# Performance work log

Measured on AMD Instinct MI355X. Metric: run time of the kernel, lower is better.

The kernel has to match this reference:

```python
import jax, jax.numpy as jnp
import numpy as np

N, NC, G, C = 80000, 8000, 16, 5
E, ES = 160000, 80000
NUM_OPS, OP_E, OP_F, CFG_F, H = 120, 32, 140, 18, 32
ALPHA = 0.2  # tf.nn.leaky_relu default slope

seg = jax.ops.segment_sum

def lrelu(x):
    return jnp.where(x >= 0, x, ALPHA * x)

def l2norm(x):
    s = jnp.sum(x * x, axis=-1, keepdims=True)
    return x * jax.lax.rsqrt(jnp.maximum(s, 1e-12))

def setup_inputs():
    k = jax.random.split(jax.random.key(0), 20)
    p = lambda i, shp, s=0.1: jax.random.normal(k[i], shp, jnp.float32) * s
    d_in = CFG_F + OP_F + OP_E  # 190: concat(config, op feats, op embed)
    d_gc = CFG_F + H            # 50: concat(config, hidden)
    return {
        'op_feats': jax.random.normal(k[0], (N, OP_F), jnp.float32),
        'config_feats': jax.random.normal(k[1], (NC, C, CFG_F), jnp.float32),
        'op_ids': jax.random.randint(k[2], (N,), 0, NUM_OPS),
        'selected': jax.random.randint(k[3], (N,), 0, 2) == 1,
        'feed_src': jax.random.randint(k[4], (E,), 0, N),
        'feed_dst': jax.random.randint(k[5], (E,), 0, N),
        'sfeed_src': jax.random.randint(k[6], (ES,), 0, N),
        'sfeed_dst': jax.random.randint(k[7], (ES,), 0, N),
        'config_src': jnp.arange(NC),
        'config_dst': jax.random.randint(k[8], (NC,), 0, N),
        'sconfig_src': jnp.arange(NC),
        'sconfig_dst': jax.random.randint(k[9], (NC,), 0, N),
        'op_gid': (jnp.arange(N) * G) // N,
        'cfg_gid': (jnp.arange(NC) * G) // NC,
        'emb': p(10, (NUM_OPS, OP_E), 1.0),
        'pre_w1': p(11, (d_in, H)), 'pre_b1': jnp.zeros((H,), jnp.float32),
        'pre_w2': p(12, (H, H)), 'pre_b2': jnp.zeros((H,), jnp.float32),
        'gc1_w1': p(13, (d_gc, H)), 'gc1_b1': jnp.zeros((H,), jnp.float32),
        'gc1_w2': p(14, (H, H)), 'gc1_b2': jnp.zeros((H,), jnp.float32),
        'gc2_w1': p(15, (d_gc, H)), 'gc2_b1': jnp.zeros((H,), jnp.float32),
        'gc2_w2': p(16, (H, H)), 'gc2_b2': jnp.zeros((H,), jnp.float32),
        'post_w1': p(17, (3 * H, H)),
        'post_w2': p(18, (H, 1)),
    }

def _mlp(x, w1, b1, w2, b2):
    return lrelu(x @ w1 + b1) @ w2 + b2

def _node_forward(nf, cf, src, dst, csrc, cdst, pre, gcs):
    # AdjacencyMultiplier('config') @ config_feats : scatter nconfig feats to ops
    cfg = 100.0 * seg(cf[csrc], cdst, num_segments=N)            # [N, C, 18]
    x = jnp.broadcast_to(nf[:, None, :], (N, C, nf.shape[-1]))   # stack over configs
    x = lrelu(_mlp(jnp.concatenate([cfg, x], -1), *pre))         # prenet + leaky_relu
    # A_hat = A + A^T + I with symmetric normalization D^-1/2 A_hat D^-1/2
    loop = jnp.arange(N)
    src_all = jnp.concatenate([src, dst, loop])
    dst_all = jnp.concatenate([dst, src, loop])
    inv = jax.lax.rsqrt(seg(jnp.ones(src_all.shape, nf.dtype), dst_all, num_segments=N))
    inv = inv[:, None, None]
    for gp in gcs:
        y = jnp.concatenate([cfg, x], -1) * inv
        y = seg(y[src_all], dst_all, num_segments=N) * inv       # A_hat_norm @ y
        x = x + lrelu(_mlp(y, *gp))                              # residual
    return x

def _forward(op_feats, config_feats, emb, pre, gc1, gc2, post_w1, post_w2,
             op_ids, selected, feed, sfeed, cfg_e, scfg_e, op_gid, cfg_gid):
    nf = jnp.concatenate([op_feats, emb[op_ids]], -1)            # [N, 172]
    x_full = _node_forward(jax.lax.stop_gradient(nf), jax.lax.stop_gradient(config_feats),
                           feed[0], feed[1], cfg_e[0], cfg_e[1], pre, (gc1, gc2))
    x_bp = _node_forward(nf, config_feats, sfeed[0], sfeed[1],
                         scfg_e[0], scfg_e[1], pre, (gc1, gc2))
    x = jnp.where(selected[:, None, None], x_bp, x_full)         # [N, C, H]
    cfg_nodes = seg(x[cfg_e[1]], cfg_e[0], num_segments=NC)      # adj_config^T @ x
    op_sum = seg(x, op_gid, num_segments=G)                      # [G, C, H]
    cnt = seg(jnp.ones((N,), x.dtype), op_gid, num_segments=G)
    op_mean = op_sum / cnt[:, None, None]
    cfg_sum = seg(cfg_nodes, cfg_gid, num_segments=G)
    feats = jnp.concatenate([op_mean, l2norm(op_sum), l2norm(cfg_sum)], -1)  # [G, C, 3H]
    return (lrelu(feats @ post_w1) @ post_w2)[..., 0]            # [G, C]

def reference(op_feats, config_feats, op_ids, selected, feed_src, feed_dst,
              sfeed_src, sfeed_dst, config_src, config_dst, sconfig_src, sconfig_dst,
              op_gid, cfg_gid, emb, pre_w1, pre_b1, pre_w2, pre_b2,
              gc1_w1, gc1_b1, gc1_w2, gc1_b2, gc2_w1, gc2_b1, gc2_w2, gc2_b2,
              post_w1, post_w2):
    return _forward(op_feats, config_feats, emb,
                    (pre_w1, pre_b1, pre_w2, pre_b2),
                    (gc1_w1, gc1_b1, gc1_w2, gc1_b2),
                    (gc2_w1, gc2_b1, gc2_w2, gc2_b2),
                    post_w1, post_w2,
                    op_ids, selected, (feed_src, feed_dst), (sfeed_src, sfeed_dst),
                    (config_src, config_dst), (sconfig_src, sconfig_dst), op_gid, cfg_gid)
```

## Files before the change

### kernel.cpp

```cpp
#include <hip/hip_runtime.h>
#include <hip/hip_bf16.h>
#include <math.h>

#define CDIV(a,b) (((a)+(b)-1)/(b))

constexpr int N_   = 80000;
constexpr int NC_  = 8000;
constexpr int G_   = 16;
constexpr int C_   = 5;
constexpr int CFGF = 18;
constexpr int OPF  = 140;
constexpr int OPE  = 32;
constexpr int H_   = 32;
constexpr int NUMOPS = 120;
constexpr int CROW = C_ * CFGF;
constexpr int XROW = C_ * H_;
constexpr float ALPHA_ = 0.2f;
constexpr int NPG = N_ / G_;
constexpr int EPG = NC_ / G_;

__device__ __forceinline__ float lrelu(float v) { return v >= 0.0f ? v : ALPHA_ * v; }

__global__ void k_nfwop(const float* __restrict__ emb, const float* __restrict__ w1,
                        const float* __restrict__ b1, float* __restrict__ nfwop) {
    int t = blockIdx.x * blockDim.x + threadIdx.x;
    if (t >= NUMOPS * H_) return;
    int op = t >> 5, h = t & 31;
    float a = b1[h];
    for (int e = 0; e < OPE; ++e)
        a = fmaf(emb[op * OPE + e], w1[(CFGF + OPF + e) * H_ + h], a);
    nfwop[t] = a;
}

__global__ void k_nfw(const float* __restrict__ opf, const int* __restrict__ op_ids,
                      const float* __restrict__ nfwop, const float* __restrict__ w1,
                      float* __restrict__ nfw) {
    int n = blockIdx.x * blockDim.x + threadIdx.x;
    if (n >= N_) return;
    float acc[H_];
    const float4* it = (const float4*)(nfwop + (size_t)op_ids[n] * H_);
    #pragma unroll
    for (int q = 0; q < 8; ++q) {
        float4 v = it[q];
        acc[4 * q + 0] = v.x; acc[4 * q + 1] = v.y; acc[4 * q + 2] = v.z; acc[4 * q + 3] = v.w;
    }
    const float4* f4 = (const float4*)(opf + (size_t)n * OPF);
    const float* wf = w1 + CFGF * H_;
    for (int kc = 0; kc < OPF / 4; ++kc) {
        float4 rv = f4[kc];
        float rs[4] = {rv.x, rv.y, rv.z, rv.w};
        #pragma unroll
        for (int j = 0; j < 4; ++j) {
            int k = kc * 4 + j;
            #pragma unroll
            for (int h = 0; h < H_; ++h) acc[h] = fmaf(rs[j], wf[k * H_ + h], acc[h]);
        }
    }
    float4* o = (float4*)(nfw + (size_t)n * H_);
    #pragma unroll
    for (int q = 0; q < 8; ++q)
        o[q] = make_float4(acc[4 * q], acc[4 * q + 1], acc[4 * q + 2], acc[4 * q + 3]);
}

__global__ void k_cfg_scatter(const float* __restrict__ cf, const int* __restrict__ cdst,
                              float* __restrict__ cfg) {
    int t = blockIdx.x * blockDim.x + threadIdx.x;
    if (t >= NC_ * CROW) return;
    int i = t / CROW, j = t - i * CROW;
    atomicAdd(&cfg[(size_t)cdst[i] * CROW + j], 100.0f * cf[t]);
}

__global__ void k_deg2(const int* __restrict__ s0, const int* __restrict__ d0, int E0,
                       const int* __restrict__ s1, const int* __restrict__ d1, int E1,
                       int* __restrict__ deg) {
    int e = blockIdx.x * blockDim.x + threadIdx.x;
    if (e < E0) {
        atomicAdd(&deg[s0[e]], 1);
        atomicAdd(&deg[d0[e]], 1);
    } else if (e < E0 + E1) {
        int e2 = e - E0;
        atomicAdd(&deg[N_ + s1[e2]], 1);
        atomicAdd(&deg[N_ + d1[e2]], 1);
    }
}

__global__ void k_inv2(const int* __restrict__ deg, float* __restrict__ inv) {
    int i = blockIdx.x * blockDim.x + threadIdx.x;
    if (i >= 2 * N_) return;
    inv[i] = 1.0f / sqrtf((float)(deg[i] + 1));
}

__global__ void k_scan1(const int* __restrict__ deg, int* __restrict__ roff, int* __restrict__ aux) {
    __shared__ int s[256];
    int t = threadIdx.x, n = blockIdx.x * 256 + t;
    int v = (n < 2 * N_) ? deg[n] : 0;
    s[t] = v; __syncthreads();
    for (int off = 1; off < 256; off <<= 1) {
        int x = (t >= off) ? s[t - off] : 0;
        __syncthreads();
        s[t] += x;
        __syncthreads();
    }
    if (n < 2 * N_) roff[n] = s[t] - v;
    if (t == 255) aux[blockIdx.x] = s[255];
}

__global__ void k_scan2(int* __restrict__ aux, int nb) {
    __shared__ int s[1024];
    int t = threadIdx.x;
    int v = (t < nb) ? aux[t] : 0;
    s[t] = v; __syncthreads();
    for (int off = 1; off < 1024; off <<= 1) {
        int x = (t >= off) ? s[t - off] : 0;
        __syncthreads();
        s[t] += x;
        __syncthreads();
    }
    if (t < nb) aux[t] = s[t] - v;
}

__global__ void k_scan3(int* __restrict__ roff, const int* __restrict__ aux,
                        int* __restrict__ cur, int total) {
    int n = blockIdx.x * blockDim.x + threadIdx.x;
    if (n < 2 * N_) {
        int r = roff[n] + aux[n >> 8];
        roff[n] = r;
        cur[n] = r;
    }
    if (n == 0) roff[2 * N_] = total;
}

__global__ void k_fill2(const int* __restrict__ s0, const int* __restrict__ d0, int E0,
                        const int* __restrict__ s1, const int* __restrict__ d1, int E1,
                        int* __restrict__ cur, int* __restrict__ col) {
    int e = blockIdx.x * blockDim.x + threadIdx.x;
    if (e < E0) {
        int s = s0[e], d = d0[e];
        col[atomicAdd(&cur[d], 1)] = s;
        col[atomicAdd(&cur[s], 1)] = d;
    } else if (e < E0 + E1) {
        int e2 = e - E0;
        int s = s1[e2], d = d1[e2];
        col[atomicAdd(&cur[N_ + d], 1)] = s;
        col[atomicAdd(&cur[N_ + s], 1)] = d;
    }
}

__global__ void k_colinv(const int* __restrict__ col, const float* __restrict__ inv,
                         int split, int total, float* __restrict__ colv) {
    int i = blockIdx.x * blockDim.x + threadIdx.x;
    if (i >= total) return;
    colv[i] = inv[(i >= split ? N_ : 0) + col[i]];
}

__global__ void k_csum_gather(const float2* __restrict__ cfg2, const float* __restrict__ inv,
                              const int* __restrict__ roff, const int* __restrict__ col,
                              const float* __restrict__ colv, float2* __restrict__ csum2) {
    int t = blockIdx.x * blockDim.x + threadIdx.x;
    if (t >= N_ * 45) return;
    int n = t / 45, j2 = t - n * 45;
    float iv = inv[n];
    float2 a = cfg2[t];
    a.x *= iv; a.y *= iv;
    int e = roff[n], p1 = roff[n + 1];
    for (; e + 1 < p1; e += 2) {
        int s0 = col[e], s1 = col[e + 1];
        float i0 = colv[e], i1 = colv[e + 1];
        float2 v0 = cfg2[(size_t)s0 * 45 + j2];
        float2 v1 = cfg2[(size_t)s1 * 45 + j2];
        a.x = fmaf(v0.x, i0, a.x); a.y = fmaf(v0.y, i0, a.y);
        a.x = fmaf(v1.x, i1, a.x); a.y = fmaf(v1.y, i1, a.y);
    }
    if (e < p1) {
        int s0 = col[e];
        float i0 = colv[e];
        float2 v0 = cfg2[(size_t)s0 * 45 + j2];
        a.x = fmaf(v0.x, i0, a.x); a.y = fmaf(v0.y, i0, a.y);
    }
    csum2[t] = a;
}

__global__ void k_pre(const float* __restrict__ cfg, const float* __restrict__ nfw,
                      const float* __restrict__ w1, const float* __restrict__ w2,
                      const float* __restrict__ b2, float* __restrict__ x) {
    int r = blockIdx.x * blockDim.x + threadIdx.x;
    if (r >= N_ * C_) return;
    int n = r / C_;
    float h1[H_];
    const float4* nf4 = (const float4*)(nfw + (size_t)n * H_);
    #pragma unroll
    for (int q = 0; q < 8; ++q) {
        float4 v = nf4[q];
        h1[4 * q + 0] = v.x; h1[4 * q + 1] = v.y; h1[4 * q + 2] = v.z; h1[4 * q + 3] = v.w;
    }
    const float2* c2 = (const float2*)(cfg + (size_t)r * CFGF);
    for (int kc = 0; kc < CFGF / 2; ++kc) {
        float2 cv = c2[kc];
        float cs[2] = {cv.x, cv.y};
        #pragma unroll
        for (int j = 0; j < 2; ++j) {
            int k = kc * 2 + j;
            #pragma unroll
            for (int h = 0; h < H_; ++h) h1[h] = fmaf(cs[j], w1[k * H_ + h], h1[h]);
        }
    }
    #pragma unroll
    for (int h = 0; h < H_; ++h) h1[h] = lrelu(h1[h]);
    float acc[H_];
    #pragma unroll
    for (int h = 0; h < H_; ++h) acc[h] = b2[h];
    #pragma unroll
    for (int k = 0; k < H_; ++k) {
        float v = h1[k];
        #pragma unroll
        for (int h = 0; h < H_; ++h) acc[h] = fmaf(v, w2[k * H_ + h], acc[h]);
    }
    float4* o = (float4*)(x + (size_t)r * H_);
    #pragma unroll
    for (int q = 0; q < 8; ++q)
        o[q] = make_float4(lrelu(acc[4 * q]), lrelu(acc[4 * q + 1]),
                           lrelu(acc[4 * q + 2]), lrelu(acc[4 * q + 3]));
}

__global__ void k_gcfused(const float4* __restrict__ xin4, const float* __restrict__ csum,
                          const float* __restrict__ inv, const int* __restrict__ roff,
                          const int* __restrict__ col, const float* __restrict__ colv,
                          const float* __restrict__ w1, const float* __restrict__ b1,
                          const float* __restrict__ w2, const float* __restrict__ b2,
                          float4* __restrict__ xout4) {
    int r = blockIdx.x * blockDim.x + threadIdx.x;
    if (r >= N_ * C_) return;
    int n = r / C_, c = r - n * C_;
    float iv = inv[n];

    float t1[H_];
    #pragma unroll
    for (int h = 0; h < H_; ++h) t1[h] = 0.0f;
    const float2* c2 = (const float2*)(csum + (size_t)r * CFGF);
    for (int kc = 0; kc < CFGF / 2; ++kc) {
        float2 cv = c2[kc];
        float cs[2] = {cv.x, cv.y};
        #pragma unroll
        for (int j = 0; j < 2; ++j) {
            int k = kc * 2 + j;
            #pragma unroll
            for (int h = 0; h < H_; ++h) t1[h] = fmaf(cs[j], w1[k * H_ + h], t1[h]);
        }
    }

    float xs[H_];
    const float4* sp = xin4 + (size_t)r * 8;
    #pragma unroll
    for (int q = 0; q < 8; ++q) {
        float4 v = sp[q];
        xs[4 * q + 0] = v.x * iv; xs[4 * q + 1] = v.y * iv;
        xs[4 * q + 2] = v.z * iv; xs[4 * q + 3] = v.w * iv;
    }
    int e = roff[n], p1 = roff[n + 1];
    for (; e + 1 < p1; e += 2) {
        int s0 = col[e], s1 = col[e + 1];
        float i0 = colv[e], i1 = colv[e + 1];
        const float4* np0 = xin4 + ((size_t)s0 * C_ + c) * 8;
        const float4* np1 = xin4 + ((size_t)s1 * C_ + c) * 8;
        #pragma unroll
        for (int q = 0; q < 8; ++q) {
            float4 v0 = np0[q];
            float4 v1 = np1[q];
            xs[4 * q + 0] = fmaf(v0.x, i0, xs[4 * q + 0]);
            xs[4 * q + 1] = fmaf(v0.y, i0, xs[4 * q + 1]);
            xs[4 * q + 2] = fmaf(v0.z, i0, xs[4 * q + 2]);
            xs[4 * q + 3] = fmaf(v0.w, i0, xs[4 * q + 3]);
            xs[4 * q + 0] = fmaf(v1.x, i1, xs[4 * q + 0]);
            xs[4 * q + 1] = fmaf(v1.y, i1, xs[4 * q + 1]);
            xs[4 * q + 2] = fmaf(v1.z, i1, xs[4 * q + 2]);
            xs[4 * q + 3] = fmaf(v1.w, i1, xs[4 * q + 3]);
        }
    }
    if (e < p1) {
        int s0 = col[e];
        float i0 = colv[e];
        const float4* np = xin4 + ((size_t)s0 * C_ + c) * 8;
        #pragma unroll
        for (int q = 0; q < 8; ++q) {
            float4 v = np[q];
            xs[4 * q + 0] = fmaf(v.x, i0, xs[4 * q + 0]);
            xs[4 * q + 1] = fmaf(v.y, i0, xs[4 * q + 1]);
            xs[4 * q + 2] = fmaf(v.z, i0, xs[4 * q + 2]);
            xs[4 * q + 3] = fmaf(v.w, i0, xs[4 * q + 3]);
        }
    }

    #pragma unroll
    for (int k = 0; k < H_; ++k) {
        float v = xs[k];
        #pragma unroll
        for (int h = 0; h < H_; ++h) t1[h] = fmaf(v, w1[(CFGF + k) * H_ + h], t1[h]);
    }
    float h1[H_];
    #pragma unroll
    for (int h = 0; h < H_; ++h) h1[h] = lrelu(fmaf(iv, t1[h], b1[h]));
    float acc[H_];
    #pragma unroll
    for (int h = 0; h < H_; ++h) acc[h] = b2[h];
    #pragma unroll
    for (int k = 0; k < H_; ++k) {
        float v = h1[k];
        #pragma unroll
        for (int h = 0; h < H_; ++h) acc[h] = fmaf(v, w2[k * H_ + h], acc[h]);
    }
    float4* o = xout4 + (size_t)r * 8;
    #pragma unroll
    for (int q = 0; q < 8; ++q) {
        float4 v = sp[q];
        v.x += lrelu(acc[4 * q + 0]); v.y += lrelu(acc[4 * q + 1]);
        v.z += lrelu(acc[4 * q + 2]); v.w += lrelu(acc[4 * q + 3]);
        o[q] = v;
    }
}

__global__ void k_opsum(const float4* __restrict__ xf4, const float4* __restrict__ xb4,
                        const int* __restrict__ sel,
                        float* __restrict__ osum, float* __restrict__ cnt) {
    __shared__ float4 ls[6 * G_ * 40];
    __shared__ float lc[6 * G_];
    for (int i = threadIdx.x; i < 6 * G_ * 40; i += blockDim.x) ls[i] = make_float4(0.f, 0.f, 0.f, 0.f);
    if (threadIdx.x < 6 * G_) lc[threadIdx.x] = 0.0f;
    __syncthreads();
    int j4 = threadIdx.x % 40, i = threadIdx.x / 40;
    const int NPB = CDIV(N_, 512);
    int start = blockIdx.x * NPB;
    int end = min(start + NPB, N_);
    if (i < 6) {
        for (int n = start + i; n < end; n += 6) {
            int g = n / NPG;
            const float4* xr = sel[n] ? xb4 : xf4;
            float4 v = xr[(size_t)n * 40 + j4];
            int o = (i * G_ + g) * 40 + j4;
            float4 cacc = ls[o];
            cacc.x += v.x; cacc.y += v.y; cacc.z += v.z; cacc.w += v.w;
            ls[o] = cacc;
            if (j4 == 0) lc[i * G_ + g] += 1.0f;
        }
    }
    __syncthreads();
    for (int idx = threadIdx.x; idx < G_ * 40; idx += blockDim.x) {
        float4 s = ls[idx];
        #pragma unroll
        for (int q = 1; q < 6; ++q) {
            float4 v = ls[q * G_ * 40 + idx];
            s.x += v.x; s.y += v.y; s.z += v.z; s.w += v.w;
        }
        int g = idx / 40, j = idx - g * 40;
        float* o = osum + (size_t)g * XROW + j * 4;
        atomicAdd(o + 0, s.x); atomicAdd(o + 1, s.y);
        atomicAdd(o + 2, s.z); atomicAdd(o + 3, s.w);
    }
    if (threadIdx.x < G_) {
        float c = 0.0f;
        #pragma unroll
        for (int q = 0; q < 6; ++q) c += lc[q * G_ + threadIdx.x];
        atomicAdd(&cnt[threadIdx.x], c);
    }
}

__global__ void k_cfgsum(const float4* __restrict__ xf4, const float4* __restrict__ xb4,
                         const int* __restrict__ sel, const int* __restrict__ cdst,
                         float* __restrict__ gsum) {
    __shared__ float4 ls[6 * G_ * 40];
    for (int i = threadIdx.x; i < 6 * G_ * 40; i += blockDim.x) ls[i] = make_float4(0.f, 0.f, 0.f, 0.f);
    __syncthreads();
    int j4 = threadIdx.x % 40, i = threadIdx.x / 40;
    const int EPB = CDIV(NC_, 64);
    int start = blockIdx.x * EPB;
    int end = min(start + EPB, NC_);
    if (i < 6) {
        for (int e = start + i; e < end; e += 6) {
            int g = e / EPG;
            int n = cdst[e];
            const float4* xr = sel[n] ? xb4 : xf4;
            float4 v = xr[(size_t)n * 40 + j4];
            int o = (i * G_ + g) * 40 + j4;
            float4 cacc = ls[o];
            cacc.x += v.x; cacc.y += v.y; cacc.z += v.z; cacc.w += v.w;
            ls[o] = cacc;
        }
    }
    __syncthreads();
    for (int idx = threadIdx.x; idx < G_ * 40; idx += blockDim.x) {
        float4 s = ls[idx];
        #pragma unroll
        for (int q = 1; q < 6; ++q) {
            float4 v = ls[q * G_ * 40 + idx];
            s.x += v.x; s.y += v.y; s.z += v.z; s.w += v.w;
        }
        int g = idx / 40, j = idx - g * 40;
        float* o = gsum + (size_t)g * XROW + j * 4;
        atomicAdd(o + 0, s.x); atomicAdd(o + 1, s.y);
        atomicAdd(o + 2, s.z); atomicAdd(o + 3, s.w);
    }
}

__global__ void k_final(const float* __restrict__ osum, const float* __restrict__ gsum,
                        const float* __restrict__ cnt, const float* __restrict__ pw1,
                        const float* __restrict__ pw2, float* __restrict__ out) {
    __shared__ float sw1[3 * H_ * H_];
    __shared__ float sw2[H_];
    for (int i = threadIdx.x; i < 3 * H_ * H_; i += blockDim.x) sw1[i] = pw1[i];
    if (threadIdx.x < H_) sw2[threadIdx.x] = pw2[threadIdx.x];
    __syncthreads();
    int t = threadIdx.x;
    if (t >= G_ * C_) return;
    int g = t / C_;
    const float* os = osum + (size_t)t * H_;
    const float* cs = gsum + (size_t)t * H_;
    float icnt = 1.0f / cnt[g];
    float a0[H_], a1[H_], a2[H_];
    float s1 = 0.0f, s2 = 0.0f;
    #pragma unroll
    for (int h = 0; h < H_; ++h) {
        float v1 = os[h], v2 = cs[h];
        a0[h] = v1 * icnt;
        a1[h] = v1; s1 = fmaf(v1, v1, s1);
        a2[h] = v2; s2 = fmaf(v2, v2, s2);
    }
    float r1 = 1.0f / sqrtf(fmaxf(s1, 1e-12f));
    float r2 = 1.0f / sqrtf(fmaxf(s2, 1e-12f));
    #pragma unroll
    for (int h = 0; h < H_; ++h) { a1[h] *= r1; a2[h] *= r2; }
    float o = 0.0f;
    #pragma unroll
    for (int h = 0; h < H_; ++h) {
        float a = 0.0f;
        #pragma unroll
        for (int k = 0; k < H_; ++k) a = fmaf(a0[k], sw1[k * H_ + h], a);
        #pragma unroll
        for (int k = 0; k < H_; ++k) a = fmaf(a1[k], sw1[(H_ + k) * H_ + h], a);
        #pragma unroll
        for (int k = 0; k < H_; ++k) a = fmaf(a2[k], sw1[(2 * H_ + k) * H_ + h], a);
        o = fmaf(lrelu(a), sw2[h], o);
    }
    out[t] = o;
}

extern "C" void kernel_launch(void* const* d_in, const int* in_sizes, int n_in,
                              void* d_out, int out_size, void* d_ws, size_t ws_size,
                              hipStream_t stream) {
    const float* op_feats     = (const float*)d_in[0];
    const float* config_feats = (const float*)d_in[1];
    const int*   op_ids       = (const int*)d_in[2];
    const int*   selected     = (const int*)d_in[3];
    const int*   feed_src     = (const int*)d_in[4];
    const int*   feed_dst     = (const int*)d_in[5];
    const int*   sfeed_src    = (const int*)d_in[6];
    const int*   sfeed_dst    = (const int*)d_in[7];
    const int*   config_dst   = (const int*)d_in[9];
    const int*   sconfig_dst  = (const int*)d_in[11];
    const float* emb          = (const float*)d_in[14];
    const float* pre_w1       = (const float*)d_in[15];
    const float* pre_b1       = (const float*)d_in[16];
    const float* pre_w2       = (const float*)d_in[17];
    const float* pre_b2       = (const float*)d_in[18];
    const float* gc_w1[2]     = {(const float*)d_in[19], (const float*)d_in[23]};
    const float* gc_b1[2]     = {(const float*)d_in[20], (const float*)d_in[24]};
    const float* gc_w2[2]     = {(const float*)d_in[21], (const float*)d_in[25]};
    const float* gc_b2[2]     = {(const float*)d_in[22], (const float*)d_in[26]};
    const float* post_w1      = (const float*)d_in[27];
    const float* post_w2      = (const float*)d_in[28];

    int E0 = in_sizes[4], E1 = in_sizes[6];
    int ecnt = 2 * (E0 + E1);

    char* ws = (char*)d_ws;
    size_t off = 0;
    auto alloc = [&](size_t bytes) { void* p = ws + off; off += (bytes + 255) & ~(size_t)255; return p; };
    float* nfw   = (float*)alloc((size_t)N_ * H_ * 4);
    float* nfwop = (float*)alloc((size_t)NUMOPS * H_ * 4);
    float* cfg   = (float*)alloc((size_t)N_ * CROW * 4);
    float* csum  = (float*)alloc((size_t)N_ * CROW * 4);
    float* xf    = (float*)alloc((size_t)N_ * XROW * 4);
    float* xb    = (float*)alloc((size_t)N_ * XROW * 4);
    float* xscr  = (float*)alloc((size_t)N_ * XROW * 4);
    float* invA  = (float*)alloc((size_t)2 * N_ * 4);
    int*   degA  = (int*)alloc((size_t)2 * N_ * 4);
    int*   roffA = (int*)alloc((size_t)(2 * N_ + 1) * 4);
    int*   curA  = (int*)alloc((size_t)2 * N_ * 4);
    int*   aux   = (int*)alloc((size_t)1024 * 4);
    int*   colA  = (int*)alloc((size_t)ecnt * 4);
    float* colvA = (float*)alloc((size_t)ecnt * 4);
    float* osum  = (float*)alloc((size_t)G_ * XROW * 4);
    float* gsum  = (float*)alloc((size_t)G_ * XROW * 4);
    float* cntb  = (float*)alloc((size_t)G_ * 4);

    const int NB1 = CDIV(2 * N_, 256);

    k_nfwop<<<CDIV(NUMOPS * H_, 256), 256, 0, stream>>>(emb, pre_w1, pre_b1, nfwop);
    k_nfw<<<CDIV(N_, 256), 256, 0, stream>>>(op_feats, op_ids, nfwop, pre_w1, nfw);

    hipMemsetAsync(degA, 0, (size_t)2 * N_ * 4, stream);
    k_deg2<<<CDIV(E0 + E1, 256), 256, 0, stream>>>(feed_src, feed_dst, E0,
                                                   sfeed_src, sfeed_dst, E1, degA);
    k_inv2<<<CDIV(2 * N_, 256), 256, 0, stream>>>(degA, invA);
    k_scan1<<<NB1, 256, 0, stream>>>(degA, roffA, aux);
    k_scan2<<<1, 1024, 0, stream>>>(aux, NB1);
    k_scan3<<<CDIV(2 * N_, 256), 256, 0, stream>>>(roffA, aux, curA, ecnt);
    k_fill2<<<CDIV(E0 + E1, 256), 256, 0, stream>>>(feed_src, feed_dst, E0,
                                                    sfeed_src, sfeed_dst, E1, curA, colA);
    k_colinv<<<CDIV(ecnt, 256), 256, 0, stream>>>(colA, invA, 2 * E0, ecnt, colvA);

    for (int p = 0; p < 2; ++p) {
        const int* cdst = p ? sconfig_dst : config_dst;
        float* x0 = p ? xb : xf;
        const float* ivp = invA + (size_t)p * N_;
        const int* roffp = roffA + (size_t)p * N_;

        hipMemsetAsync(cfg, 0, (size_t)N_ * CROW * 4, stream);
        k_cfg_scatter<<<CDIV(NC_ * CROW, 256), 256, 0, stream>>>(config_feats, cdst, cfg);
        k_csum_gather<<<CDIV(N_ * 45, 256), 256, 0, stream>>>((const float2*)cfg, ivp, roffp,
                                                              colA, colvA, (float2*)csum);
        k_pre<<<CDIV(N_ * C_, 256), 256, 0, stream>>>(cfg, nfw, pre_w1, pre_w2, pre_b2, x0);

        k_gcfused<<<CDIV(N_ * C_, 256), 256, 0, stream>>>((const float4*)x0, csum, ivp, roffp,
                                                          colA, colvA, gc_w1[0], gc_b1[0],
                                                          gc_w2[0], gc_b2[0], (float4*)xscr);
        k_gcfused<<<CDIV(N_ * C_, 256), 256, 0, stream>>>((const float4*)xscr, csum, ivp, roffp,
                                                          colA, colvA, gc_w1[1], gc_b1[1],
                                                          gc_w2[1], gc_b2[1], (float4*)x0);
    }

    hipMemsetAsync(osum, 0, (size_t)(2 * G_ * XROW + G_) * 4, stream);
    k_opsum<<<512, 256, 0, stream>>>((const float4*)xf, (const float4*)xb, selected, osum, cntb);
    k_cfgsum<<<64, 256, 0, stream>>>((const float4*)xf, (const float4*)xb, selected,
                                     config_dst, gsum);
    k_final<<<1, 128, 0, stream>>>(osum, gsum, cntb, post_w1, post_w2, (float*)d_out);
}
```

Measured before the change: 694.9 us.

## Store node hidden states config-major so gcfused gathers stay in one plane

Hidden state arrays change from [N][C][H] to [C][N][H] layout, and k_gcfused now runs on a 2D grid with blockIdx.y selecting the config. Neighbor gathers for a given config then hit a contiguous 10 MB plane rather than striding across all configs, which is meant to improve cache locality for the random edge gathers. k_pre, k_opsum and k_cfgsum are updated to the new indexing. The csum reads stay node-major and are now strided per thread, which may cost some coalescing.

```diff
diff --git a/kernel.cpp b/kernel.cpp
--- a/kernel.cpp
+++ b/kernel.cpp
@@ -185,7 +185,7 @@
                       const float* __restrict__ b2, float* __restrict__ x) {
     int r = blockIdx.x * blockDim.x + threadIdx.x;
     if (r >= N_ * C_) return;
-    int n = r / C_;
+    int n = r / C_, c = r - n * C_;
     float h1[H_];
     const float4* nf4 = (const float4*)(nfw + (size_t)n * H_);
     #pragma unroll
@@ -215,7 +215,7 @@
         #pragma unroll
         for (int h = 0; h < H_; ++h) acc[h] = fmaf(v, w2[k * H_ + h], acc[h]);
     }
-    float4* o = (float4*)(x + (size_t)r * H_);
+    float4* o = (float4*)x + ((size_t)c * N_ + n) * 8;
     #pragma unroll
     for (int q = 0; q < 8; ++q)
         o[q] = make_float4(lrelu(acc[4 * q]), lrelu(acc[4 * q + 1]),
@@ -228,15 +228,15 @@
                           const float* __restrict__ w1, const float* __restrict__ b1,
                           const float* __restrict__ w2, const float* __restrict__ b2,
                           float4* __restrict__ xout4) {
-    int r = blockIdx.x * blockDim.x + threadIdx.x;
-    if (r >= N_ * C_) return;
-    int n = r / C_, c = r - n * C_;
+    int n = blockIdx.x * blockDim.x + threadIdx.x;
+    int c = blockIdx.y;
+    if (n >= N_) return;
     float iv = inv[n];
 
     float t1[H_];
     #pragma unroll
     for (int h = 0; h < H_; ++h) t1[h] = 0.0f;
-    const float2* c2 = (const float2*)(csum + (size_t)r * CFGF);
+    const float2* c2 = (const float2*)(csum + ((size_t)n * C_ + c) * CFGF);
     for (int kc = 0; kc < CFGF / 2; ++kc) {
         float2 cv = c2[kc];
         float cs[2] = {cv.x, cv.y};
@@ -248,8 +248,9 @@
         }
     }
 
+    const float4* plane = xin4 + (size_t)c * N_ * 8;
     float xs[H_];
-    const float4* sp = xin4 + (size_t)r * 8;
+    const float4* sp = plane + (size_t)n * 8;
     #pragma unroll
     for (int q = 0; q < 8; ++q) {
         float4 v = sp[q];
@@ -260,8 +261,8 @@
     for (; e + 1 < p1; e += 2) {
         int s0 = col[e], s1 = col[e + 1];
         float i0 = colv[e], i1 = colv[e + 1];
-        const float4* np0 = xin4 + ((size_t)s0 * C_ + c) * 8;
-        const float4* np1 = xin4 + ((size_t)s1 * C_ + c) * 8;
+        const float4* np0 = plane + (size_t)s0 * 8;
+        const float4* np1 = plane + (size_t)s1 * 8;
         #pragma unroll
         for (int q = 0; q < 8; ++q) {
             float4 v0 = np0[q];
@@ -279,7 +280,7 @@
     if (e < p1) {
         int s0 = col[e];
         float i0 = colv[e];
-        const float4* np = xin4 + ((size_t)s0 * C_ + c) * 8;
+        const float4* np = plane + (size_t)s0 * 8;
         #pragma unroll
         for (int q = 0; q < 8; ++q) {
             float4 v = np[q];
@@ -308,7 +309,7 @@
         #pragma unroll
         for (int h = 0; h < H_; ++h) acc[h] = fmaf(v, w2[k * H_ + h], acc[h]);
     }
-    float4* o = xout4 + (size_t)r * 8;
+    float4* o = xout4 + (size_t)c * N_ * 8 + (size_t)n * 8;
     #pragma unroll
     for (int q = 0; q < 8; ++q) {
         float4 v = sp[q];
@@ -327,6 +328,8 @@
     if (threadIdx.x < 6 * G_) lc[threadIdx.x] = 0.0f;
     __syncthreads();
     int j4 = threadIdx.x % 40, i = threadIdx.x / 40;
+    int cpl = j4 >> 3, q = j4 & 7;
+    size_t poff = ((size_t)cpl * N_) * 8 + q;
     const int NPB = CDIV(N_, 512);
     int start = blockIdx.x * NPB;
     int end = min(start + NPB, N_);
@@ -334,7 +337,7 @@
         for (int n = start + i; n < end; n += 6) {
             int g = n / NPG;
             const float4* xr = sel[n] ? xb4 : xf4;
-            float4 v = xr[(size_t)n * 40 + j4];
+            float4 v = xr[poff + (size_t)n * 8];
             int o = (i * G_ + g) * 40 + j4;
             float4 cacc = ls[o];
             cacc.x += v.x; cacc.y += v.y; cacc.z += v.z; cacc.w += v.w;
@@ -346,8 +349,8 @@
     for (int idx = threadIdx.x; idx < G_ * 40; idx += blockDim.x) {
         float4 s = ls[idx];
         #pragma unroll
-        for (int q = 1; q < 6; ++q) {
-            float4 v = ls[q * G_ * 40 + idx];
+        for (int qq = 1; qq < 6; ++qq) {
+            float4 v = ls[qq * G_ * 40 + idx];
             s.x += v.x; s.y += v.y; s.z += v.z; s.w += v.w;
         }
         int g = idx / 40, j = idx - g * 40;
@@ -358,7 +361,7 @@
     if (threadIdx.x < G_) {
         float c = 0.0f;
         #pragma unroll
-        for (int q = 0; q < 6; ++q) c += lc[q * G_ + threadIdx.x];
+        for (int qq = 0; qq < 6; ++qq) c += lc[qq * G_ + threadIdx.x];
         atomicAdd(&cnt[threadIdx.x], c);
     }
 }
@@ -370,6 +373,8 @@
     for (int i = threadIdx.x; i < 6 * G_ * 40; i += blockDim.x) ls[i] = make_float4(0.f, 0.f, 0.f, 0.f);
     __syncthreads();
     int j4 = threadIdx.x % 40, i = threadIdx.x / 40;
+    int cpl = j4 >> 3, q = j4 & 7;
+    size_t poff = ((size_t)cpl * N_) * 8 + q;
     const int EPB = CDIV(NC_, 64);
     int start = blockIdx.x * EPB;
     int end = min(start + EPB, NC_);
@@ -378,7 +383,7 @@
             int g = e / EPG;
             int n = cdst[e];
             const float4* xr = sel[n] ? xb4 : xf4;
-            float4 v = xr[(size_t)n * 40 + j4];
+            float4 v = xr[poff + (size_t)n * 8];
             int o = (i * G_ + g) * 40 + j4;
             float4 cacc = ls[o];
             cacc.x += v.x; cacc.y += v.y; cacc.z += v.z; cacc.w += v.w;
@@ -389,8 +394,8 @@
     for (int idx = threadIdx.x; idx < G_ * 40; idx += blockDim.x) {
         float4 s = ls[idx];
         #pragma unroll
-        for (int q = 1; q < 6; ++q) {
-            float4 v = ls[q * G_ * 40 + idx];
+        for (int qq = 1; qq < 6; ++qq) {
+            float4 v = ls[qq * G_ * 40 + idx];
             s.x += v.x; s.y += v.y; s.z += v.z; s.w += v.w;
         }
         int g = idx / 40, j = idx - g * 40;
@@ -492,6 +497,7 @@
     float* cntb  = (float*)alloc((size_t)G_ * 4);
 
     const int NB1 = CDIV(2 * N_, 256);
+    const dim3 gcGrid(CDIV(N_, 256), C_);
 
     k_nfwop<<<CDIV(NUMOPS * H_, 256), 256, 0, stream>>>(emb, pre_w1, pre_b1, nfwop);
     k_nfw<<<CDIV(N_, 256), 256, 0, stream>>>(op_feats, op_ids, nfwop, pre_w1, nfw);
@@ -519,12 +525,12 @@
                                                               colA, colvA, (float2*)csum);
         k_pre<<<CDIV(N_ * C_, 256), 256, 0, stream>>>(cfg, nfw, pre_w1, pre_w2, pre_b2, x0);
 
-        k_gcfused<<<CDIV(N_ * C_, 256), 256, 0, stream>>>((const float4*)x0, csum, ivp, roffp,
-                                                          colA, colvA, gc_w1[0], gc_b1[0],
-                                                          gc_w2[0], gc_b2[0], (float4*)xscr);
-        k_gcfused<<<CDIV(N_ * C_, 256), 256, 0, stream>>>((const float4*)xscr, csum, ivp, roffp,
-                                                          colA, colvA, gc_w1[1], gc_b1[1],
-                                                          gc_w2[1], gc_b2[1], (float4*)x0);
+        k_gcfused<<<gcGrid, 256, 0, stream>>>((const float4*)x0, csum, ivp, roffp,
+                                              colA, colvA, gc_w1[0], gc_b1[0],
+                                              gc_w2[0], gc_b2[0], (float4*)xscr);
+        k_gcfused<<<gcGrid, 256, 0, stream>>>((const float4*)xscr, csum, ivp, roffp,
+                                              colA, colvA, gc_w1[1], gc_b1[1],
+                                              gc_w2[1], gc_b2[1], (float4*)x0);
     }
 
     hipMemsetAsync(osum, 0, (size_t)(2 * G_ * XROW + G_) * 4, stream);
```

After: 782.5 us. 12.6% more time.

## Split graph-conv rows across two threads with shared-memory exchange

Applied to the files above, without the earlier changes.

Each graph-conv row is now handled by two threads, each computing 16 of the 32 hidden outputs. The aggregated neighbour features and the first-layer activations are swapped through a padded shared-memory tile with block barriers. The goal is to halve per-thread register arrays, raising occupancy and doubling the threads doing the memory-bound neighbour gather. In exchange it adds barriers and shared-memory traffic, and every neighbour's column and weight index is loaded by both threads of a pair.

```diff
diff --git a/kernel.cpp b/kernel.cpp
--- a/kernel.cpp
+++ b/kernel.cpp
@@ -15,6 +15,7 @@
 constexpr int NUMOPS = 120;
 constexpr int CROW = C_ * CFGF;
 constexpr int XROW = C_ * H_;
+constexpr int NR   = N_ * C_;
 constexpr float ALPHA_ = 0.2f;
 constexpr int NPG = N_ / G_;
 constexpr int EPG = NC_ / G_;
@@ -184,7 +185,7 @@
                       const float* __restrict__ w1, const float* __restrict__ w2,
                       const float* __restrict__ b2, float* __restrict__ x) {
     int r = blockIdx.x * blockDim.x + threadIdx.x;
-    if (r >= N_ * C_) return;
+    if (r >= NR) return;
     int n = r / C_;
     float h1[H_];
     const float4* nf4 = (const float4*)(nfw + (size_t)n * H_);
@@ -222,36 +223,40 @@
                            lrelu(acc[4 * q + 2]), lrelu(acc[4 * q + 3]));
 }
 
-__global__ void k_gcfused(const float4* __restrict__ xin4, const float* __restrict__ csum,
-                          const float* __restrict__ inv, const int* __restrict__ roff,
-                          const int* __restrict__ col, const float* __restrict__ colv,
-                          const float* __restrict__ w1, const float* __restrict__ b1,
-                          const float* __restrict__ w2, const float* __restrict__ b2,
-                          float4* __restrict__ xout4) {
-    int r = blockIdx.x * blockDim.x + threadIdx.x;
-    if (r >= N_ * C_) return;
+__global__ __launch_bounds__(256) void k_gcsplit(
+        const float4* __restrict__ xin4, const float* __restrict__ csum,
+        const float* __restrict__ inv, const int* __restrict__ roff,
+        const int* __restrict__ col, const float* __restrict__ colv,
+        const float* __restrict__ w1, const float* __restrict__ b1,
+        const float* __restrict__ w2, const float* __restrict__ b2,
+        float4* __restrict__ xout4) {
+    __shared__ float sx[128][33];
+    int tid = threadIdx.x;
+    int half = tid >> 7, rl = tid & 127;
+    int r = blockIdx.x * 128 + rl;
     int n = r / C_, c = r - n * C_;
     float iv = inv[n];
-
-    float t1[H_];
-    #pragma unroll
-    for (int h = 0; h < H_; ++h) t1[h] = 0.0f;
+    int h0 = half * 16;
+
+    float t1[16];
+    #pragma unroll
+    for (int j = 0; j < 16; ++j) t1[j] = 0.0f;
     const float2* c2 = (const float2*)(csum + (size_t)r * CFGF);
     for (int kc = 0; kc < CFGF / 2; ++kc) {
         float2 cv = c2[kc];
         float cs[2] = {cv.x, cv.y};
         #pragma unroll
-        for (int j = 0; j < 2; ++j) {
-            int k = kc * 2 + j;
+        for (int jj = 0; jj < 2; ++jj) {
+            int k = kc * 2 + jj;
             #pragma unroll
-            for (int h = 0; h < H_; ++h) t1[h] = fmaf(cs[j], w1[k * H_ + h], t1[h]);
-        }
-    }
-
-    float xs[H_];
-    const float4* sp = xin4 + (size_t)r * 8;
-    #pragma unroll
-    for (int q = 0; q < 8; ++q) {
+            for (int j = 0; j < 16; ++j) t1[j] = fmaf(cs[jj], w1[k * H_ + h0 + j], t1[j]);
+        }
+    }
+
+    float xs[16];
+    const float4* sp = xin4 + (size_t)r * 8 + half * 4;
+    #pragma unroll
+    for (int q = 0; q < 4; ++q) {
         float4 v = sp[q];
         xs[4 * q + 0] = v.x * iv; xs[4 * q + 1] = v.y * iv;
         xs[4 * q + 2] = v.z * iv; xs[4 * q + 3] = v.w * iv;
@@ -260,10 +265,10 @@
     for (; e + 1 < p1; e += 2) {
         int s0 = col[e], s1 = col[e + 1];
         float i0 = colv[e], i1 = colv[e + 1];
-        const float4* np0 = xin4 + ((size_t)s0 * C_ + c) * 8;
-        const float4* np1 = xin4 + ((size_t)s1 * C_ + c) * 8;
-        #pragma unroll
-        for (int q = 0; q < 8; ++q) {
+        const float4* np0 = xin4 + ((size_t)s0 * C_ + c) * 8 + half * 4;
+        const float4* np1 = xin4 + ((size_t)s1 * C_ + c) * 8 + half * 4;
+        #pragma unroll
+        for (int q = 0; q < 4; ++q) {
             float4 v0 = np0[q];
             float4 v1 = np1[q];
             xs[4 * q + 0] = fmaf(v0.x, i0, xs[4 * q + 0]);
@@ -279,9 +284,9 @@
     if (e < p1) {
         int s0 = col[e];
         float i0 = colv[e];
-        const float4* np = xin4 + ((size_t)s0 * C_ + c) * 8;
-        #pragma unroll
-        for (int q = 0; q < 8; ++q) {
+        const float4* np = xin4 + ((size_t)s0 * C_ + c) * 8 + half * 4;
+        #pragma unroll
+        for (int q = 0; q < 4; ++q) {
             float4 v = np[q];
             xs[4 * q + 0] = fmaf(v.x, i0, xs[4 * q + 0]);
             xs[4 * q + 1] = fmaf(v.y, i0, xs[4 * q + 1]);
@@ -289,28 +294,36 @@
             xs[4 * q + 3] = fmaf(v.w, i0, xs[4 * q + 3]);
         }
     }
+    #pragma unroll
+    for (int j = 0; j < 16; ++j) sx[rl][h0 + j] = xs[j];
+    __syncthreads();
 
     #pragma unroll
     for (int k = 0; k < H_; ++k) {
-        float v = xs[k];
-        #pragma unroll
-        for (int h = 0; h < H_; ++h) t1[h] = fmaf(v, w1[(CFGF + k) * H_ + h], t1[h]);
-    }
-    float h1[H_];
-    #pragma unroll
-    for (int h = 0; h < H_; ++h) h1[h] = lrelu(fmaf(iv, t1[h], b1[h]));
-    float acc[H_];
-    #pragma unroll
-    for (int h = 0; h < H_; ++h) acc[h] = b2[h];
+        float v = sx[rl][k];
+        #pragma unroll
+        for (int j = 0; j < 16; ++j) t1[j] = fmaf(v, w1[(CFGF + k) * H_ + h0 + j], t1[j]);
+    }
+    float h1[16];
+    #pragma unroll
+    for (int j = 0; j < 16; ++j) h1[j] = lrelu(fmaf(iv, t1[j], b1[h0 + j]));
+    __syncthreads();
+    #pragma unroll
+    for (int j = 0; j < 16; ++j) sx[rl][h0 + j] = h1[j];
+    __syncthreads();
+
+    float acc[16];
+    #pragma unroll
+    for (int j = 0; j < 16; ++j) acc[j] = b2[h0 + j];
     #pragma unroll
     for (int k = 0; k < H_; ++k) {
-        float v = h1[k];
-        #pragma unroll
-        for (int h = 0; h < H_; ++h) acc[h] = fmaf(v, w2[k * H_ + h], acc[h]);
-    }
-    float4* o = xout4 + (size_t)r * 8;
-    #pragma unroll
-    for (int q = 0; q < 8; ++q) {
+        float v = sx[rl][k];
+        #pragma unroll
+        for (int j = 0; j < 16; ++j) acc[j] = fmaf(v, w2[k * H_ + h0 + j], acc[j]);
+    }
+    float4* o = xout4 + (size_t)r * 8 + half * 4;
+    #pragma unroll
+    for (int q = 0; q < 4; ++q) {
         float4 v = sp[q];
         v.x += lrelu(acc[4 * q + 0]); v.y += lrelu(acc[4 * q + 1]);
         v.z += lrelu(acc[4 * q + 2]); v.w += lrelu(acc[4 * q + 3]);
@@ -517,14 +530,14 @@
         k_cfg_scatter<<<CDIV(NC_ * CROW, 256), 256, 0, stream>>>(config_feats, cdst, cfg);
         k_csum_gather<<<CDIV(N_ * 45, 256), 256, 0, stream>>>((const float2*)cfg, ivp, roffp,
                                                               colA, colvA, (float2*)csum);
-        k_pre<<<CDIV(N_ * C_, 256), 256, 0, stream>>>(cfg, nfw, pre_w1, pre_w2, pre_b2, x0);
-
-        k_gcfused<<<CDIV(N_ * C_, 256), 256, 0, stream>>>((const float4*)x0, csum, ivp, roffp,
-                                                          colA, colvA, gc_w1[0], gc_b1[0],
-                                                          gc_w2[0], gc_b2[0], (float4*)xscr);
-        k_gcfused<<<CDIV(N_ * C_, 256), 256, 0, stream>>>((const float4*)xscr, csum, ivp, roffp,
-                                                          colA, colvA, gc_w1[1], gc_b1[1],
-                                                          gc_w2[1], gc_b2[1], (float4*)x0);
+        k_pre<<<CDIV(NR, 256), 256, 0, stream>>>(cfg, nfw, pre_w1, pre_w2, pre_b2, x0);
+
+        k_gcsplit<<<NR / 128, 256, 0, stream>>>((const float4*)x0, csum, ivp, roffp,
+                                                colA, colvA, gc_w1[0], gc_b1[0],
+                                                gc_w2[0], gc_b2[0], (float4*)xscr);
+        k_gcsplit<<<NR / 128, 256, 0, stream>>>((const float4*)xscr, csum, ivp, roffp,
+                                                colA, colvA, gc_w1[1], gc_b1[1],
+                                                gc_w2[1], gc_b2[1], (float4*)x0);
     }
 
     hipMemsetAsync(osum, 0, (size_t)(2 * G_ * XROW + G_) * 4, stream);
```

Measured after the change: 1.079 ms. +55.3%, slower.
